# Performance work log

Measured on AMD Instinct MI355X. Metric: run time of the kernel, lower is better.

The kernel has to match this reference:

```python
import jax, jax.numpy as jnp
import numpy as np

I_T = 0.5       # IoU threshold self.I_t
GAMMA = 2.0     # focal loss gamma
EPS = 1e-7      # focal loss eps clamp
BS, P, C_IN = 8, 2048, 512


def pairwise_iou(b):
    # b: (bs, P, 4) xyxy -> (bs, P, P), same math as torchvision box_iou (no +1)
    area = (b[..., 2] - b[..., 0]) * (b[..., 3] - b[..., 1])
    lt = jnp.maximum(b[:, :, None, :2], b[:, None, :, :2])
    rb = jnp.minimum(b[:, :, None, 2:], b[:, None, :, 2:])
    wh = jnp.clip(rb - lt, 0.0, None)
    inter = wh[..., 0] * wh[..., 1]
    return inter / (area[:, :, None] + area[:, None, :] - inter)


def assign_labels_weights(pre_score, labels, rois):
    # Vectorized, order-faithful version of the per-batch/per-class python loop.
    # Selected seeds per class c: proposals with pre_score[...,c] > 0.5 if more than
    # one, else the single argmax proposal (torch code falls back when k<=1).
    # Sequential `_I > old` running max over (c, j) in ascending order is equivalent
    # to a global first-occurrence argmax (strict >), so per-class max + running
    # compare with earlier-class tie preference reproduces it exactly.
    bs, Pn = pre_score.shape[0], pre_score.shape[1]
    iou = pairwise_iou(rois)                      # (bs, P, P)
    run_I = jnp.full((bs, Pn), -1.0, pre_score.dtype)
    run_w = jnp.ones((bs, Pn), pre_score.dtype)
    hits = []
    for c in range(3):
        s = pre_score[:, :, c]                    # (bs, P)
        th = s > 0.5
        cnt = th.sum(-1)
        onehot = jnp.arange(Pn)[None, :] == jnp.argmax(s, -1)[:, None]
        sel = jnp.where((cnt > 1)[:, None], th, onehot)
        sel = sel & (labels[:, c] != 0)[:, None]  # skip classes absent from image
        masked = jnp.where(sel[:, None, :], iou, -2.0)  # (bs, P, P)
        val = masked.max(-1)                      # best IoU vs any seed of class c
        jidx = masked.argmax(-1)
        cand_x = jnp.take_along_axis(s, jidx, axis=1)
        better = val > run_I
        run_w = jnp.where(better, cand_x, run_w)
        run_I = jnp.where(better, val, run_I)
        hits.append(val > I_T)
    hit = jnp.stack(hits, -1)                     # (bs, P, 3)
    bg = (~hit.any(-1))[..., None]
    y = jnp.concatenate([hit.astype(pre_score.dtype), bg.astype(pre_score.dtype)], -1)
    return y, run_w


def icr_forward(inputs, fc_w, fc_b, pre_score, labels, rois, num):
    bs = inputs.shape[0] // num
    xr = inputs @ fc_w + fc_b                     # (bs*P, 4)
    logit = jax.nn.softmax(xr.reshape(bs, num, 4), -1)
    ps = jax.lax.stop_gradient(pre_score)         # .clone().detach()
    lb = jax.lax.stop_gradient(labels)
    y, w = assign_labels_weights(ps, lb, rois)
    y = y.reshape(bs * num, 4)
    w = w.reshape(bs * num, 1)
    # FocalLoss(gamma=2, mode='none')
    p = jnp.clip(jax.nn.softmax(xr, -1), EPS, 1.0 - EPS)
    fl = -y * jnp.log(p) * (1.0 - p) ** GAMMA
    imbalance = y.sum(0)                          # (4,)
    loss = (w * fl / (imbalance + 1e-7)).reshape(bs, num, 4)
    lab = lb.at[:, 3].set(1.0)[:, None, :]        # lab[:,0,3]=1
    w_ = 10.0 * jnp.exp(logit) * (1.0 - lab) + lab
    loss = (loss * w_).sum() / bs
    return logit, loss


def setup_inputs():
    key = jax.random.key(0)
    k = jax.random.split(key, 6)
    inputs = jax.random.normal(k[0], (BS * P, C_IN), jnp.float32)
    fc_w = jax.random.normal(k[1], (C_IN, 4), jnp.float32) * 0.02
    fc_b = jnp.zeros((4,), jnp.float32)
    pre_score = jax.random.uniform(k[2], (BS, P, 4), dtype=jnp.float32)
    labels = (jax.random.uniform(k[3], (BS, 4)) < 0.5).astype(jnp.float32)
    labels = labels.at[:, 3].set(0.0)
    xy = jax.random.uniform(k[4], (BS, P, 2), dtype=jnp.float32) * 448.0
    wh = jax.random.uniform(k[5], (BS, P, 2), dtype=jnp.float32) * 63.0 + 1.0
    rois = jnp.concatenate([xy, xy + wh], -1)     # valid xyxy boxes in 512x512
    return {"inputs": inputs, "fc_w": fc_w, "fc_b": fc_b, "pre_score": pre_score,
            "labels": labels, "rois": rois, "num": P}


def reference(inputs, fc_w, fc_b, pre_score, labels, rois, num):
    return icr_forward(inputs, fc_w, fc_b, pre_score, labels, rois, num)
```

## Files before the change

### kernel.cpp

```cpp
#include <hip/hip_runtime.h>

#define BSZ 8
#define PN  2048
#define CIN 512
#define CAP 2048
#define NW  16


__global__ __launch_bounds__(256) void k_front(
    const float* __restrict__ inp, const float* __restrict__ fcw,
    const float* __restrict__ fcb, const float* __restrict__ ps,
    const float* __restrict__ labels, const float* __restrict__ rois,
    float* __restrict__ logit, float* __restrict__ accum,
    int* __restrict__ meta, float* __restrict__ sList,
    float4* __restrict__ roiList)
{
  const int t = threadIdx.x;
  if (blockIdx.x >= 24) {
    const int gw   = (((int)blockIdx.x - 24) * 256 + t) >> 6;
    const int lane = t & 63;
    const int kb   = lane << 2;
    const float4 wa0 = *(const float4*)(fcw + (kb + 0) * 4);
    const float4 wa1 = *(const float4*)(fcw + (kb + 1) * 4);
    const float4 wa2 = *(const float4*)(fcw + (kb + 2) * 4);
    const float4 wa3 = *(const float4*)(fcw + (kb + 3) * 4);
    const float4 wb0 = *(const float4*)(fcw + (256 + kb + 0) * 4);
    const float4 wb1 = *(const float4*)(fcw + (256 + kb + 1) * 4);
    const float4 wb2 = *(const float4*)(fcw + (256 + kb + 2) * 4);
    const float4 wb3 = *(const float4*)(fcw + (256 + kb + 3) * 4);
    const float4 bias = *(const float4*)fcb;
    #pragma unroll
    for (int rr = 0; rr < 4; ++rr) {
      const int r = (gw << 2) + rr;
      const float* row = inp + r * CIN;
      const float4 xa = *(const float4*)(row + kb);
      const float4 xb = *(const float4*)(row + 256 + kb);
      float a0 = xa.x*wa0.x + xa.y*wa1.x + xa.z*wa2.x + xa.w*wa3.x
               + xb.x*wb0.x + xb.y*wb1.x + xb.z*wb2.x + xb.w*wb3.x;
      float a1 = xa.x*wa0.y + xa.y*wa1.y + xa.z*wa2.y + xa.w*wa3.y
               + xb.x*wb0.y + xb.y*wb1.y + xb.z*wb2.y + xb.w*wb3.y;
      float a2 = xa.x*wa0.z + xa.y*wa1.z + xa.z*wa2.z + xa.w*wa3.z
               + xb.x*wb0.z + xb.y*wb1.z + xb.z*wb2.z + xb.w*wb3.z;
      float a3 = xa.x*wa0.w + xa.y*wa1.w + xa.z*wa2.w + xa.w*wa3.w
               + xb.x*wb0.w + xb.y*wb1.w + xb.z*wb2.w + xb.w*wb3.w;
      #pragma unroll
      for (int off = 32; off; off >>= 1) {
        a0 += __shfl_xor(a0, off); a1 += __shfl_xor(a1, off);
        a2 += __shfl_xor(a2, off); a3 += __shfl_xor(a3, off);
      }
      if (lane == 0) {
        a0 += bias.x; a1 += bias.y; a2 += bias.z; a3 += bias.w;
        const float m  = fmaxf(fmaxf(a0, a1), fmaxf(a2, a3));
        const float e0 = expf(a0 - m), e1 = expf(a1 - m);
        const float e2 = expf(a2 - m), e3 = expf(a3 - m);
        const float inv = 1.0f / (e0 + e1 + e2 + e3);
        float4 o; o.x = e0*inv; o.y = e1*inv; o.z = e2*inv; o.w = e3*inv;
        *(float4*)(logit + r * 4) = o;
      }
    }
    return;
  }

  const int bc = blockIdx.x;
  if (bc == 0 && t < 12) accum[t] = 0.0f;
  const int b = bc / 3;
  const int c = bc % 3;
  const int j0 = t * 8;

  float sv[8];
  int   flg = 0, cnt = 0;
  float vmax = -1e30f;
  int   jmax = 0;
  #pragma unroll
  for (int m = 0; m < 8; ++m) {
    const float s = ps[(b * PN + j0 + m) * 4 + c];
    sv[m] = s;
    if (s > 0.5f) { flg |= 1 << m; ++cnt; }
    if (s > vmax) { vmax = s; jmax = j0 + m; }
  }

  __shared__ float lv[256];
  __shared__ int   lj[256];
  __shared__ int   pre[256];
  lv[t] = vmax; lj[t] = jmax; pre[t] = cnt;
  __syncthreads();
  for (int off = 128; off > 0; off >>= 1) {
    if (t < off) {
      const float v2 = lv[t + off]; const int j2 = lj[t + off];
      if (v2 > lv[t] || (v2 == lv[t] && j2 < lj[t])) { lv[t] = v2; lj[t] = j2; }
    }
    __syncthreads();
  }
  for (int off = 1; off < 256; off <<= 1) {
    const int add = (t >= off) ? pre[t - off] : 0;
    __syncthreads();
    pre[t] += add;
    __syncthreads();
  }
  const int  totalTh = pre[255];
  const int  excl    = pre[t] - cnt;
  const int  jArg    = lj[0];
  const bool lab     = labels[b * 4 + c] != 0.0f;
  const int  L    = (!lab) ? 0 : ((totalTh > 1) ? totalTh : 1);
  const int  Lpad = (L + 7) & ~7;

  __shared__ float4 lastRoi;
  __shared__ float  lastS;
  float4* dstR = roiList + bc * CAP;
  float*  dstS = sList   + bc * CAP;
  const float4* rb = ((const float4*)rois) + b * PN;

  if (lab) {
    if (totalTh > 1) {
      int pos = excl;
      #pragma unroll
      for (int m = 0; m < 8; ++m) {
        if (flg & (1 << m)) {
          const float4 r = rb[j0 + m];
          dstR[pos] = r; dstS[pos] = sv[m];
          if (pos == L - 1) { lastRoi = r; lastS = sv[m]; }
          ++pos;
        }
      }
    } else if (t == (jArg >> 3)) {
      const float4 r = rb[jArg];
      dstR[0] = r; dstS[0] = sv[jArg & 7];
      lastRoi = r; lastS = sv[jArg & 7];
    }
  }
  __syncthreads();
  if (t < Lpad - L) { dstR[L + t] = lastRoi; dstS[L + t] = lastS; }
  if (t == 0) meta[bc] = Lpad;
}

__global__ __launch_bounds__(1024, 4) void k_assign(
    const float* __restrict__ rois, const int* __restrict__ meta,
    const float4* __restrict__ roiList, const float* __restrict__ sList,
    const float* __restrict__ logit, const float* __restrict__ labels,
    float* __restrict__ accum, float* __restrict__ loss)
{
  const int blk  = blockIdx.x;
  const int t    = threadIdx.x;
  const int lane = t & 63;
  const int wv   = t >> 6;
  const int b    = blk >> 5;
  const int it   = blk & 31;

  __shared__ __align__(16) float4 sroi[2048];
  __shared__ float smn[NW][64];
  __shared__ float smd[NW][64];
  __shared__ int   smp[NW][64];

  const int i = (it << 6) + lane;
  const float4 ri = ((const float4*)rois)[b * PN + i];
  const float areai = (ri.z - ri.x) * (ri.w - ri.y);

  auto upd = [&](float& n, float& d, int& p, const float4 rj, const int pos) {
    const float aj = (rj.z - rj.x) * (rj.w - rj.y);
    const float lx = fmaxf(ri.x, rj.x), ly = fmaxf(ri.y, rj.y);
    const float rx = fminf(ri.z, rj.z), ry = fminf(ri.w, rj.w);
    const float ww = fmaxf(rx - lx, 0.0f), hh = fmaxf(ry - ly, 0.0f);
    const float inter = ww * hh;
    const float uni   = areai + aj - inter;
    if (inter * d > n * uni) { n = inter; d = uni; p = pos; }
  };

  float BNf[3], BDf[3]; int BPf[3];

  for (int c = 0; c < 3; ++c) {
    const int cnt = meta[b * 3 + c];
    const float4* src = roiList + (b * 3 + c) * CAP;
    if (t < cnt)        sroi[t]        = src[t];
    if (t + 1024 < cnt) sroi[t + 1024] = src[t + 1024];
    __syncthreads();

    const int C  = (((cnt + 15) >> 4) + 7) & ~7;
    const int g0 = wv * C;
    int g1 = g0 + C; if (g1 > cnt) g1 = cnt;
    float nA = -2.0f, dA = 1.0f, nB = -2.0f, dB = 1.0f;
    int   pA = 0, pB = 0;
    for (int g = g0; g < g1; g += 4) {
      const float4 r0 = sroi[g],     r1 = sroi[g + 1];
      const float4 r2 = sroi[g + 2], r3 = sroi[g + 3];
      upd(nA, dA, pA, r0, g);
      upd(nB, dB, pB, r2, g + 2);
      upd(nA, dA, pA, r1, g + 1);
      upd(nB, dB, pB, r3, g + 3);
    }
    const float tB = nB * dA, tA = nA * dB;
    if (tB > tA || (tB == tA && pB < pA)) { nA = nB; dA = dB; pA = pB; }

    smn[wv][lane] = nA; smd[wv][lane] = dA; smp[wv][lane] = pA;
    __syncthreads();
    if (wv == 0) {
      float bn = nA, bd = dA; int bp = pA;
      #pragma unroll 1
      for (int w2 = 1; w2 < NW; ++w2) {
        const float n = smn[w2][lane];
        const float d = smd[w2][lane];
        const int   p = smp[w2][lane];
        if (n * bd > bn * d) { bn = n; bd = d; bp = p; }
      }
      BNf[c] = bn; BDf[c] = bd; BPf[c] = bp;
    }
    __syncthreads();
  }

  if (wv != 0) return;

  const int gi = b * PN + i;
  float v[3], sc[3];
  #pragma unroll
  for (int c = 0; c < 3; ++c) {
    v[c]  = BNf[c] / BDf[c];
    sc[c] = sList[(b * 3 + c) * CAP + BPf[c]];
  }
  float runI = -1.0f, runw = 1.0f;
  if (v[0] > runI) { runw = sc[0]; runI = v[0]; }
  if (v[1] > runI) { runw = sc[1]; runI = v[1]; }
  if (v[2] > runI) { runw = sc[2]; runI = v[2]; }
  const float y0 = (v[0] > 0.5f) ? 1.0f : 0.0f;
  const float y1 = (v[1] > 0.5f) ? 1.0f : 0.0f;
  const float y2 = (v[2] > 0.5f) ? 1.0f : 0.0f;
  const float y3 = (y0 + y1 + y2 == 0.0f) ? 1.0f : 0.0f;

  const float4 lg = ((const float4*)logit)[gi];
  const float lb0 = labels[b * 4 + 0];
  const float lb1 = labels[b * 4 + 1];
  const float lb2 = labels[b * 4 + 2];

  auto term = [&](const float l, const float yv, const float labv) -> float {
    const float p  = fminf(fmaxf(l, 1e-7f), 1.0f - 1e-7f);
    const float om = 1.0f - p;
    const float fl = -yv * logf(p) * om * om;
    const float wl = 10.0f * expf(l) * (1.0f - labv) + labv;
    return runw * fl * wl;
  };
  float s[8];
  s[0] = term(lg.x, y0, lb0); s[1] = term(lg.y, y1, lb1);
  s[2] = term(lg.z, y2, lb2); s[3] = term(lg.w, y3, 1.0f);
  s[4] = y0; s[5] = y1; s[6] = y2; s[7] = y3;

  #pragma unroll
  for (int k = 0; k < 8; ++k)
    #pragma unroll
    for (int off = 32; off; off >>= 1) s[k] += __shfl_xor(s[k], off);

  if (lane == 0) {
    #pragma unroll
    for (int k = 0; k < 8; ++k) atomicAdd(&accum[k], s[k]);
    __threadfence();
    const int ticket = __hip_atomic_fetch_add((int*)(accum + 8), 1,
                        __ATOMIC_ACQ_REL, __HIP_MEMORY_SCOPE_AGENT);
    if (ticket == 255) {
      float L = 0.0f;
      #pragma unroll
      for (int c = 0; c < 4; ++c) {
        const float num = __hip_atomic_load(accum + c,
                            __ATOMIC_RELAXED, __HIP_MEMORY_SCOPE_AGENT);
        const float den = __hip_atomic_load(accum + 4 + c,
                            __ATOMIC_RELAXED, __HIP_MEMORY_SCOPE_AGENT);
        L += num / (den + 1e-7f);
      }
      loss[0] = L * 0.125f;
    }
  }
}

extern "C" void kernel_launch(void* const* d_in, const int* in_sizes, int n_in,
                              void* d_out, int out_size, void* d_ws, size_t ws_size,
                              hipStream_t stream)
{
  (void)in_sizes; (void)n_in; (void)out_size; (void)ws_size;
  const float* inp    = (const float*)d_in[0];
  const float* fcw    = (const float*)d_in[1];
  const float* fcb    = (const float*)d_in[2];
  const float* ps     = (const float*)d_in[3];
  const float* labels = (const float*)d_in[4];
  const float* rois   = (const float*)d_in[5];
  float* out = (float*)d_out;

  char* ws = (char*)d_ws;
  float*  accum   = (float*) (ws);
  int*    meta    = (int*)   (ws + 64);
  float*  sList   = (float*) (ws + 1024);
  float4* roiL    = (float4*)(ws + 394240);

  k_front <<<1048, 256,  0, stream>>>(inp, fcw, fcb, ps, labels, rois,
                                      out, accum, meta, sList, roiL);
  k_assign<<<256,  1024, 0, stream>>>(rois, meta, roiL, sList, out, labels,
                                      accum, out + BSZ * PN * 4);
}
```

Baseline: 136.7 us.

## Split assign kernel into 512 smaller blocks with 32 proposals and 16 seed chunks

```diff
diff --git a/kernel.cpp b/kernel.cpp
--- a/kernel.cpp
+++ b/kernel.cpp
@@ -4,7 +4,6 @@
 #define PN  2048
 #define CIN 512
 #define CAP 2048
-#define NW  16
 
 
 __global__ __launch_bounds__(256) void k_front(
@@ -133,25 +132,28 @@
   if (t == 0) meta[bc] = Lpad;
 }
 
-__global__ __launch_bounds__(1024, 4) void k_assign(
+__global__ __launch_bounds__(512, 8) void k_assign(
     const float* __restrict__ rois, const int* __restrict__ meta,
     const float4* __restrict__ roiList, const float* __restrict__ sList,
     const float* __restrict__ logit, const float* __restrict__ labels,
     float* __restrict__ accum, float* __restrict__ loss)
 {
-  const int blk  = blockIdx.x;
-  const int t    = threadIdx.x;
-  const int lane = t & 63;
-  const int wv   = t >> 6;
-  const int b    = blk >> 5;
-  const int it   = blk & 31;
-
-  __shared__ __align__(16) float4 sroi[2048];
-  __shared__ float smn[NW][64];
-  __shared__ float smd[NW][64];
-  __shared__ int   smp[NW][64];
-
-  const int i = (it << 6) + lane;
+  const int blk   = blockIdx.x;
+  const int t     = threadIdx.x;
+  const int lane  = t & 63;
+  const int wv    = t >> 6;
+  const int l32   = lane & 31;
+  const int chunk = (wv << 1) | (lane >> 5);
+  const int b     = blk & 7;
+  const int it    = blk >> 3;
+  const int i     = (it << 5) + l32;
+
+  __shared__ __align__(16) char ldsraw[32768];
+  float4* sroi = (float4*)ldsraw;
+  float*  smn  = (float*)ldsraw;
+  float*  smd  = (float*)(ldsraw + 2048);
+  int*    smp  = (int*)  (ldsraw + 4096);
+
   const float4 ri = ((const float4*)rois)[b * PN + i];
   const float areai = (ri.z - ri.x) * (ri.w - ri.y);
 
@@ -167,15 +169,16 @@
 
   float BNf[3], BDf[3]; int BPf[3];
 
+  #pragma unroll
   for (int c = 0; c < 3; ++c) {
     const int cnt = meta[b * 3 + c];
     const float4* src = roiList + (b * 3 + c) * CAP;
-    if (t < cnt)        sroi[t]        = src[t];
-    if (t + 1024 < cnt) sroi[t + 1024] = src[t + 1024];
+    for (int idx = t; idx < cnt; idx += 512)
+      sroi[idx] = src[idx];
     __syncthreads();
 
     const int C  = (((cnt + 15) >> 4) + 7) & ~7;
-    const int g0 = wv * C;
+    const int g0 = chunk * C;
     int g1 = g0 + C; if (g1 > cnt) g1 = cnt;
     float nA = -2.0f, dA = 1.0f, nB = -2.0f, dB = 1.0f;
     int   pA = 0, pB = 0;
@@ -190,15 +193,17 @@
     const float tB = nB * dA, tA = nA * dB;
     if (tB > tA || (tB == tA && pB < pA)) { nA = nB; dA = dB; pA = pB; }
 
-    smn[wv][lane] = nA; smd[wv][lane] = dA; smp[wv][lane] = pA;
-    __syncthreads();
-    if (wv == 0) {
+    __syncthreads();
+    smn[chunk * 32 + l32] = nA;
+    smd[chunk * 32 + l32] = dA;
+    smp[chunk * 32 + l32] = pA;
+    __syncthreads();
+    if (wv == 0 && lane < 32) {
       float bn = nA, bd = dA; int bp = pA;
-      #pragma unroll 1
-      for (int w2 = 1; w2 < NW; ++w2) {
-        const float n = smn[w2][lane];
-        const float d = smd[w2][lane];
-        const int   p = smp[w2][lane];
+      for (int k = 1; k < 16; ++k) {
+        const float n = smn[k * 32 + l32];
+        const float d = smd[k * 32 + l32];
+        const int   p = smp[k * 32 + l32];
         if (n * bd > bn * d) { bn = n; bd = d; bp = p; }
       }
       BNf[c] = bn; BDf[c] = bd; BPf[c] = bp;
@@ -208,51 +213,51 @@
 
   if (wv != 0) return;
 
-  const int gi = b * PN + i;
-  float v[3], sc[3];
-  #pragma unroll
-  for (int c = 0; c < 3; ++c) {
-    v[c]  = BNf[c] / BDf[c];
-    sc[c] = sList[(b * 3 + c) * CAP + BPf[c]];
-  }
-  float runI = -1.0f, runw = 1.0f;
-  if (v[0] > runI) { runw = sc[0]; runI = v[0]; }
-  if (v[1] > runI) { runw = sc[1]; runI = v[1]; }
-  if (v[2] > runI) { runw = sc[2]; runI = v[2]; }
-  const float y0 = (v[0] > 0.5f) ? 1.0f : 0.0f;
-  const float y1 = (v[1] > 0.5f) ? 1.0f : 0.0f;
-  const float y2 = (v[2] > 0.5f) ? 1.0f : 0.0f;
-  const float y3 = (y0 + y1 + y2 == 0.0f) ? 1.0f : 0.0f;
-
-  const float4 lg = ((const float4*)logit)[gi];
-  const float lb0 = labels[b * 4 + 0];
-  const float lb1 = labels[b * 4 + 1];
-  const float lb2 = labels[b * 4 + 2];
-
-  auto term = [&](const float l, const float yv, const float labv) -> float {
-    const float p  = fminf(fmaxf(l, 1e-7f), 1.0f - 1e-7f);
-    const float om = 1.0f - p;
-    const float fl = -yv * logf(p) * om * om;
-    const float wl = 10.0f * expf(l) * (1.0f - labv) + labv;
-    return runw * fl * wl;
-  };
-  float s[8];
-  s[0] = term(lg.x, y0, lb0); s[1] = term(lg.y, y1, lb1);
-  s[2] = term(lg.z, y2, lb2); s[3] = term(lg.w, y3, 1.0f);
-  s[4] = y0; s[5] = y1; s[6] = y2; s[7] = y3;
-
+  float s[8] = {0.f, 0.f, 0.f, 0.f, 0.f, 0.f, 0.f, 0.f};
+  if (lane < 32) {
+    const int gi = b * PN + i;
+    float v[3], sc[3];
+    #pragma unroll
+    for (int c = 0; c < 3; ++c) {
+      v[c]  = BNf[c] / BDf[c];
+      sc[c] = sList[(b * 3 + c) * CAP + BPf[c]];
+    }
+    float runI = -1.0f, runw = 1.0f;
+    if (v[0] > runI) { runw = sc[0]; runI = v[0]; }
+    if (v[1] > runI) { runw = sc[1]; runI = v[1]; }
+    if (v[2] > runI) { runw = sc[2]; runI = v[2]; }
+    const float y0 = (v[0] > 0.5f) ? 1.0f : 0.0f;
+    const float y1 = (v[1] > 0.5f) ? 1.0f : 0.0f;
+    const float y2 = (v[2] > 0.5f) ? 1.0f : 0.0f;
+    const float y3 = (y0 + y1 + y2 == 0.0f) ? 1.0f : 0.0f;
+
+    const float4 lg = ((const float4*)logit)[gi];
+    const float lb0 = labels[b * 4 + 0];
+    const float lb1 = labels[b * 4 + 1];
+    const float lb2 = labels[b * 4 + 2];
+
+    auto term = [&](const float l, const float yv, const float labv) -> float {
+      const float p  = fminf(fmaxf(l, 1e-7f), 1.0f - 1e-7f);
+      const float om = 1.0f - p;
+      const float fl = -yv * logf(p) * om * om;
+      const float wl = 10.0f * expf(l) * (1.0f - labv) + labv;
+      return runw * fl * wl;
+    };
+    s[0] = term(lg.x, y0, lb0); s[1] = term(lg.y, y1, lb1);
+    s[2] = term(lg.z, y2, lb2); s[3] = term(lg.w, y3, 1.0f);
+    s[4] = y0; s[5] = y1; s[6] = y2; s[7] = y3;
+  }
   #pragma unroll
   for (int k = 0; k < 8; ++k)
     #pragma unroll
     for (int off = 32; off; off >>= 1) s[k] += __shfl_xor(s[k], off);
 
+  if (lane < 8) atomicAdd(&accum[lane], s[lane]);
+  __threadfence();
   if (lane == 0) {
-    #pragma unroll
-    for (int k = 0; k < 8; ++k) atomicAdd(&accum[k], s[k]);
-    __threadfence();
     const int ticket = __hip_atomic_fetch_add((int*)(accum + 8), 1,
                         __ATOMIC_ACQ_REL, __HIP_MEMORY_SCOPE_AGENT);
-    if (ticket == 255) {
+    if (ticket == 511) {
       float L = 0.0f;
       #pragma unroll
       for (int c = 0; c < 4; ++c) {
@@ -286,8 +291,8 @@
   float*  sList   = (float*) (ws + 1024);
   float4* roiL    = (float4*)(ws + 394240);
 
-  k_front <<<1048, 256,  0, stream>>>(inp, fcw, fcb, ps, labels, rois,
-                                      out, accum, meta, sList, roiL);
-  k_assign<<<256,  1024, 0, stream>>>(rois, meta, roiL, sList, out, labels,
-                                      accum, out + BSZ * PN * 4);
+  k_front <<<1048, 256, 0, stream>>>(inp, fcw, fcb, ps, labels, rois,
+                                     out, accum, meta, sList, roiL);
+  k_assign<<<512,  512, 0, stream>>>(rois, meta, roiL, sList, out, labels,
+                                     accum, out + BSZ * PN * 4);
 }
```

After: 133.7 us. 1.02x faster.

## Split assign kernel per class across blocks and add separate loss reduction kernel

Applied to the files above, without the earlier changes.

```diff
diff --git a/kernel.cpp b/kernel.cpp
--- a/kernel.cpp
+++ b/kernel.cpp
@@ -133,27 +133,38 @@
   if (t == 0) meta[bc] = Lpad;
 }
 
-__global__ __launch_bounds__(1024, 4) void k_assign(
+__global__ __launch_bounds__(1024, 8) void k_assign(
     const float* __restrict__ rois, const int* __restrict__ meta,
-    const float4* __restrict__ roiList, const float* __restrict__ sList,
-    const float* __restrict__ logit, const float* __restrict__ labels,
-    float* __restrict__ accum, float* __restrict__ loss)
+    const float4* __restrict__ roiList,
+    float* __restrict__ pbn, float* __restrict__ pbd, int* __restrict__ pbp)
 {
   const int blk  = blockIdx.x;
+  const int bc   = blk >> 5;
+  const int it   = blk & 31;
+  const int b    = bc / 3;
   const int t    = threadIdx.x;
   const int lane = t & 63;
   const int wv   = t >> 6;
-  const int b    = blk >> 5;
-  const int it   = blk & 31;
 
   __shared__ __align__(16) float4 sroi[2048];
-  __shared__ float smn[NW][64];
-  __shared__ float smd[NW][64];
-  __shared__ int   smp[NW][64];
-
+  float* smn = (float*)sroi;
+  float* smd = (float*)sroi + 1024;
+  int*   smp = (int*)((float*)sroi + 2048);
+
+  const int cnt   = meta[bc];
+  const int obase = bc * PN + (it << 6);
+  if (cnt == 0) {
+    if (t < 64) { pbn[obase + t] = -2.0f; pbd[obase + t] = 1.0f; pbp[obase + t] = 0; }
+    return;
+  }
+
+  const float4* src = roiList + bc * CAP;
+  for (int idx = t; idx < cnt; idx += 1024)
+    sroi[idx] = src[idx];
   const int i = (it << 6) + lane;
   const float4 ri = ((const float4*)rois)[b * PN + i];
   const float areai = (ri.z - ri.x) * (ri.w - ri.y);
+  __syncthreads();
 
   auto upd = [&](float& n, float& d, int& p, const float4 rj, const int pos) {
     const float aj = (rj.z - rj.x) * (rj.w - rj.y);
@@ -165,55 +176,59 @@
     if (inter * d > n * uni) { n = inter; d = uni; p = pos; }
   };
 
-  float BNf[3], BDf[3]; int BPf[3];
-
-  for (int c = 0; c < 3; ++c) {
-    const int cnt = meta[b * 3 + c];
-    const float4* src = roiList + (b * 3 + c) * CAP;
-    if (t < cnt)        sroi[t]        = src[t];
-    if (t + 1024 < cnt) sroi[t + 1024] = src[t + 1024];
-    __syncthreads();
-
-    const int C  = (((cnt + 15) >> 4) + 7) & ~7;
-    const int g0 = wv * C;
-    int g1 = g0 + C; if (g1 > cnt) g1 = cnt;
-    float nA = -2.0f, dA = 1.0f, nB = -2.0f, dB = 1.0f;
-    int   pA = 0, pB = 0;
-    for (int g = g0; g < g1; g += 4) {
-      const float4 r0 = sroi[g],     r1 = sroi[g + 1];
-      const float4 r2 = sroi[g + 2], r3 = sroi[g + 3];
-      upd(nA, dA, pA, r0, g);
-      upd(nB, dB, pB, r2, g + 2);
-      upd(nA, dA, pA, r1, g + 1);
-      upd(nB, dB, pB, r3, g + 3);
-    }
-    const float tB = nB * dA, tA = nA * dB;
-    if (tB > tA || (tB == tA && pB < pA)) { nA = nB; dA = dB; pA = pB; }
-
-    smn[wv][lane] = nA; smd[wv][lane] = dA; smp[wv][lane] = pA;
-    __syncthreads();
-    if (wv == 0) {
-      float bn = nA, bd = dA; int bp = pA;
-      #pragma unroll 1
-      for (int w2 = 1; w2 < NW; ++w2) {
-        const float n = smn[w2][lane];
-        const float d = smd[w2][lane];
-        const int   p = smp[w2][lane];
-        if (n * bd > bn * d) { bn = n; bd = d; bp = p; }
-      }
-      BNf[c] = bn; BDf[c] = bd; BPf[c] = bp;
-    }
-    __syncthreads();
-  }
-
-  if (wv != 0) return;
-
-  const int gi = b * PN + i;
+  const int C  = (((cnt + 15) >> 4) + 7) & ~7;
+  const int g0 = wv * C;
+  int g1 = g0 + C; if (g1 > cnt) g1 = cnt;
+  float nA = -2.0f, dA = 1.0f, nB = -2.0f, dB = 1.0f;
+  int   pA = 0, pB = 0;
+  for (int g = g0; g < g1; g += 4) {
+    const float4 r0 = sroi[g],     r1 = sroi[g + 1];
+    const float4 r2 = sroi[g + 2], r3 = sroi[g + 3];
+    upd(nA, dA, pA, r0, g);
+    upd(nB, dB, pB, r2, g + 2);
+    upd(nA, dA, pA, r1, g + 1);
+    upd(nB, dB, pB, r3, g + 3);
+  }
+  const float tB = nB * dA, tA = nA * dB;
+  if (tB > tA || (tB == tA && pB < pA)) { nA = nB; dA = dB; pA = pB; }
+
+  __syncthreads();
+  smn[wv * 64 + lane] = nA;
+  smd[wv * 64 + lane] = dA;
+  smp[wv * 64 + lane] = pA;
+  __syncthreads();
+  if (wv == 0) {
+    float bn = nA, bd = dA; int bp = pA;
+    for (int k = 1; k < NW; ++k) {
+      const float n = smn[k * 64 + lane];
+      const float d = smd[k * 64 + lane];
+      const int   p = smp[k * 64 + lane];
+      if (n * bd > bn * d) { bn = n; bd = d; bp = p; }
+    }
+    pbn[obase + lane] = bn;
+    pbd[obase + lane] = bd;
+    pbp[obase + lane] = bp;
+  }
+}
+
+__global__ __launch_bounds__(256) void k_back(
+    const float* __restrict__ pbn, const float* __restrict__ pbd,
+    const int* __restrict__ pbp, const float* __restrict__ sList,
+    const float* __restrict__ logit, const float* __restrict__ labels,
+    float* __restrict__ accum, float* __restrict__ loss)
+{
+  const int t  = threadIdx.x;
+  const int gi = blockIdx.x * 256 + t;
+  const int b  = gi >> 11;
+  const int i  = gi & (PN - 1);
+
   float v[3], sc[3];
   #pragma unroll
   for (int c = 0; c < 3; ++c) {
-    v[c]  = BNf[c] / BDf[c];
-    sc[c] = sList[(b * 3 + c) * CAP + BPf[c]];
+    const int o = (b * 3 + c) * PN + i;
+    const float n = pbn[o], d = pbd[o];
+    v[c]  = n / d;
+    sc[c] = sList[(b * 3 + c) * CAP + pbp[o]];
   }
   float runI = -1.0f, runw = 1.0f;
   if (v[0] > runI) { runw = sc[0]; runI = v[0]; }
@@ -246,13 +261,22 @@
     #pragma unroll
     for (int off = 32; off; off >>= 1) s[k] += __shfl_xor(s[k], off);
 
-  if (lane == 0) {
+  __shared__ float red[4][8];
+  const int wv = t >> 6;
+  if ((t & 63) == 0)
     #pragma unroll
-    for (int k = 0; k < 8; ++k) atomicAdd(&accum[k], s[k]);
+    for (int k = 0; k < 8; ++k) red[wv][k] = s[k];
+  __syncthreads();
+  if (t < 8) {
+    const float sum = red[0][t] + red[1][t] + red[2][t] + red[3][t];
+    atomicAdd(&accum[t], sum);
+  }
+  __syncthreads();
+  if (t == 0) {
     __threadfence();
     const int ticket = __hip_atomic_fetch_add((int*)(accum + 8), 1,
                         __ATOMIC_ACQ_REL, __HIP_MEMORY_SCOPE_AGENT);
-    if (ticket == 255) {
+    if (ticket == 63) {
       float L = 0.0f;
       #pragma unroll
       for (int c = 0; c < 4; ++c) {
@@ -285,9 +309,13 @@
   int*    meta    = (int*)   (ws + 64);
   float*  sList   = (float*) (ws + 1024);
   float4* roiL    = (float4*)(ws + 394240);
+  float*  pbn     = (float*) (ws + 1180672);
+  float*  pbd     = (float*) (ws + 1573888);
+  int*    pbp     = (int*)   (ws + 1967104);
 
   k_front <<<1048, 256,  0, stream>>>(inp, fcw, fcb, ps, labels, rois,
                                       out, accum, meta, sList, roiL);
-  k_assign<<<256,  1024, 0, stream>>>(rois, meta, roiL, sList, out, labels,
-                                      accum, out + BSZ * PN * 4);
+  k_assign<<<768,  1024, 0, stream>>>(rois, meta, roiL, pbn, pbd, pbp);
+  k_back  <<<64,   256,  0, stream>>>(pbn, pbd, pbp, sList, out, labels, accum,
+                                      out + BSZ * PN * 4);
 }
```

After: 117.6 us. -14.0%, faster.
